# Performance work log

Hardware: AMD Instinct MI355X
Metric: run time of the kernel (lower is better)

The kernel has to match this reference:

```python
import jax, jax.numpy as jnp
import numpy as np

NUM_HEADS = 16

def setup_inputs() -> dict:
    key = jax.random.key(0)
    k1, k2, k3, k4 = jax.random.split(key, 4)
    B, S, D = 4, 4096, 2048
    scale = 1.0 / np.sqrt(D)
    return {
        "x": jax.random.normal(k1, (B, S, D), dtype=jnp.float32),
        "W_q": jax.random.normal(k2, (D, D), dtype=jnp.float32) * scale,
        "W_kv": jax.random.normal(k3, (D, D), dtype=jnp.float32) * scale,
        "W_o": jax.random.normal(k4, (D, D), dtype=jnp.float32) * scale,
    }

def _l2_normalize_complex(z):
    # torch.norm(z, dim=-1, keepdim=True) for complex: sqrt(sum |z|^2)
    n = jnp.sqrt(jnp.sum(jnp.abs(z) ** 2, axis=-1, keepdims=True))
    return z / n

def reference(x, W_q, W_kv, W_o):
    B, S, D = x.shape
    H = NUM_HEADS
    hd = D // H
    # Linear (no bias), torch convention: x @ W.T
    q = (x @ W_q.T).reshape(B, S, H, hd)
    kv = (x @ W_kv.T).reshape(B, S, H, hd)
    # HRR binding: FFT along head dim
    qf = jnp.fft.fft(q, axis=-1)
    kvf = jnp.fft.fft(kv, axis=-1)
    qf = _l2_normalize_complex(qf)
    kvf = _l2_normalize_complex(kvf)
    # causal=True: cumulative sum of bound key-values over sequence
    kvf = jnp.cumsum(kvf, axis=1)
    qv = qf * kvf
    values_hat = jnp.fft.ifft(qv, axis=-1).real.astype(x.dtype)
    values_hat = values_hat.reshape(B, S, D)
    return values_hat @ W_o.T
```

## Files before the change

### kernel.cpp

```cpp
#include <hip/hip_runtime.h>
#include <hip/hip_bf16.h>


typedef unsigned short u16;
typedef unsigned int u32;
typedef __attribute__((ext_vector_type(8))) short short8;
typedef __attribute__((ext_vector_type(4))) float f32x4;

__device__ __forceinline__ float bf2f(u16 u) {
  u32 x = ((u32)u) << 16;
  float f; __builtin_memcpy(&f, &x, 4); return f;
}
__device__ __forceinline__ u16 f2bf(float f) {
  __hip_bfloat16 h = __float2bfloat16(f);
  u16 u; __builtin_memcpy(&u, &h, 2); return u;
}
__device__ __forceinline__ u32 pack2(float a, float b) {
  return (u32)f2bf(a) | ((u32)f2bf(b) << 16);
}

#define GLD16(gp, lp)                                                        \
  __builtin_amdgcn_global_load_lds(                                          \
      (const __attribute__((address_space(1))) void*)(gp),                   \
      (__attribute__((address_space(3))) void*)(lp), 16, 0, 0)

__device__ __forceinline__ unsigned ldsoff(const void* p) {
  return (unsigned)(size_t)(const __attribute__((address_space(3))) char*)p;
}

#define DSR(dst, ad, im)                                                     \
  asm volatile("ds_read_b128 %0, %1 offset:%c2"                              \
               : "=v"(dst) : "v"(ad), "i"(im))

#define MM2(ACCE, X0, X1, Y0, Y1)                                            \
  ACCE = __builtin_amdgcn_mfma_f32_16x16x32_bf16(X0, Y0, ACCE, 0, 0, 0);     \
  ACCE = __builtin_amdgcn_mfma_f32_16x16x32_bf16(X1, Y1, ACCE, 0, 0, 0)

template <int EPI>
__global__ __launch_bounds__(512, 2) void gemm256(
    const u16* __restrict__ A, const u16* __restrict__ B, void* __restrict__ C,
    int N, int K) {
  __shared__ alignas(1024) char smem[131072];
  const int NT = K >> 6;
  const int ntn = N >> 8;
  const int nwg = gridDim.x;
  int wg = blockIdx.x;
  wg = (wg & 7) * (nwg >> 3) + (wg >> 3);
  const int bm = wg / ntn, bn = wg % ntn;
  const long rowBase = (long)bm << 8, colBase = (long)bn << 8;

  const int tid = threadIdx.x;
  const int w = tid >> 6, lane = tid & 63;
  const int quad = lane >> 4, l16 = lane & 15;
  const int wm = w >> 2, wn = w & 3;

  const int grow = w * 8 + (lane >> 3);
  const int gcol = ((lane & 7) * 8) ^ ((lane >> 4) << 4);
  const long voff = (long)grow * K + gcol;
  const u16* Abase = A + rowBase * (long)K;
  const u16* Bbase = B + colBase * (long)K;
  char* ldsA = smem;
  char* ldsB = smem + 65536;

#define STG_A(v, h)                                                          \
  do {                                                                       \
    char* d_ = ldsA + (((v)&1) << 15) + ((h) << 14) + (w << 10);             \
    GLD16(Abase + ((h) * 128L) * K + (long)(v) * 64 + voff, d_);             \
    GLD16(Abase + ((h) * 128L + 64) * K + (long)(v) * 64 + voff, d_ + 8192); \
  } while (0)
#define STG_B(v, h)                                                          \
  do {                                                                       \
    char* d_ = ldsB + (((v)&1) << 15) + ((h) << 14) + (w << 10);             \
    GLD16(Bbase + ((h) * 128L) * K + (long)(v) * 64 + voff, d_);             \
    GLD16(Bbase + ((h) * 128L + 64) * K + (long)(v) * 64 + voff, d_ + 8192); \
  } while (0)

  const int cb0 = (quad << 4) ^ (((l16 >> 1) & 3) << 5);
  const unsigned bA0 = ldsoff(ldsA + (wm * 128 + l16) * 128) + cb0;
  const unsigned bA1 = bA0 ^ 64;
  const unsigned bB0 = ldsoff(ldsB + (wn * 64 + l16) * 128) + cb0;
  const unsigned bB1 = bB0 ^ 64;

  short8 aL[8], aH[8], bl[4], bh[4];
  f32x4 acc[8][4] = {};

  STG_A(0, 0); STG_A(0, 1); STG_B(0, 0); STG_B(0, 1);
  STG_B(1, 0); STG_B(1, 1);
  asm volatile("s_waitcnt vmcnt(4)");
  __builtin_amdgcn_s_barrier();
  __builtin_amdgcn_sched_barrier(0);

#define Q0_BODY                                                              \
  _Pragma("unroll") for (int i = 0; i < 4; i++)                              \
    _Pragma("unroll") for (int j = 0; j < 2; j++) {                          \
      MM2(acc[i][j], aL[2*i], aL[2*i+1], bl[2*j], bl[2*j+1]);                \
    }
#define Q1_BODY                                                              \
  _Pragma("unroll") for (int i = 0; i < 4; i++)                              \
    _Pragma("unroll") for (int j = 0; j < 2; j++) {                          \
      MM2(acc[i][j+2], aL[2*i], aL[2*i+1], bh[2*j], bh[2*j+1]);              \
    }
#define Q2_BODY                                                              \
  _Pragma("unroll") for (int i = 0; i < 4; i++)                              \
    _Pragma("unroll") for (int j = 0; j < 2; j++) {                          \
      MM2(acc[i+4][j], aH[2*i], aH[2*i+1], bl[2*j], bl[2*j+1]);              \
    }
#define Q3_BODY                                                              \
  _Pragma("unroll") for (int i = 0; i < 4; i++)                              \
    _Pragma("unroll") for (int j = 0; j < 2; j++) {                          \
      MM2(acc[i+4][j+2], aH[2*i], aH[2*i+1], bh[2*j], bh[2*j+1]);            \
    }

#define RUN_TILE(uu, SA_, SB_, WAITSTMT)                                     \
  do {                                                                       \
    const unsigned bsel = ((uu) & 1) << 15;                                  \
    const unsigned aA0 = bA0 ^ bsel, aA1 = bA1 ^ bsel;                       \
    const unsigned aB0 = bB0 ^ bsel, aB1 = bB1 ^ bsel;                       \
                   \
    _Pragma("unroll") for (int i = 0; i < 4; i++) {                          \
      DSR(aL[2*i],   aA0, i * 2048);                                         \
      DSR(aL[2*i+1], aA1, i * 2048);                                         \
    }                                                                        \
    _Pragma("unroll") for (int j = 0; j < 2; j++) {                          \
      DSR(bl[2*j],   aB0, j * 2048);                                         \
      DSR(bl[2*j+1], aB1, j * 2048);                                         \
    }                                                                        \
    _Pragma("unroll") for (int j = 0; j < 2; j++) {                          \
      DSR(bh[2*j],   aB0, (j + 2) * 2048);                                   \
      DSR(bh[2*j+1], aB1, (j + 2) * 2048);                                   \
    }                                                                        \
    _Pragma("unroll") for (int i = 0; i < 4; i++) {                          \
      DSR(aH[2*i],   aA0, (i + 4) * 2048);                                   \
      DSR(aH[2*i+1], aA1, (i + 4) * 2048);                                   \
    }                                                                        \
    if (SA_) { STG_A((uu) + 1, 0); STG_A((uu) + 1, 1); }                     \
                       \
    asm volatile("s_waitcnt lgkmcnt(12)");                                   \
    __builtin_amdgcn_sched_barrier(0);                                       \
    __builtin_amdgcn_s_setprio(1);                                           \
    Q0_BODY                                                                  \
    __builtin_amdgcn_s_setprio(0);                                           \
                                   \
    asm volatile("s_waitcnt lgkmcnt(8)");                                    \
    __builtin_amdgcn_sched_barrier(0);                                       \
    __builtin_amdgcn_s_setprio(1);                                           \
    Q1_BODY                                                                  \
    __builtin_amdgcn_s_setprio(0);                                           \
    \
                       \
    __builtin_amdgcn_s_barrier();                                            \
    __builtin_amdgcn_sched_barrier(0);                                       \
    if (SB_) { STG_B((uu) + 2, 0); STG_B((uu) + 2, 1); }                     \
                                                          \
    asm volatile("s_waitcnt lgkmcnt(0)");                                    \
    __builtin_amdgcn_sched_barrier(0);                                       \
    __builtin_amdgcn_s_setprio(1);                                           \
    Q2_BODY                                                                  \
    Q3_BODY                                                                  \
    __builtin_amdgcn_s_setprio(0);                                           \
    WAITSTMT;                                                                \
    __builtin_amdgcn_s_barrier();                                            \
    __builtin_amdgcn_sched_barrier(0);                                       \
  } while (0)

  for (int u = 0; u < NT - 2; ++u) {
    RUN_TILE(u, true, true, asm volatile("s_waitcnt vmcnt(4)"));
  }
  RUN_TILE(NT - 2, true, false, asm volatile("s_waitcnt vmcnt(0)"));
  RUN_TILE(NT - 1, false, false, (void)0);
#undef RUN_TILE
#undef Q0_BODY
#undef Q1_BODY
#undef Q2_BODY
#undef Q3_BODY
#undef STG_A
#undef STG_B

  asm volatile("" ::: "memory");

  float scl[8][4];
#pragma unroll
  for (int i = 0; i < 8; i++)
#pragma unroll
    for (int r = 0; r < 4; r++) scl[i][r] = 1.0f;

  if (EPI == 2) {
    float* ssb = (float*)smem;
    __syncthreads();
#pragma unroll
    for (int i = 0; i < 8; i++)
#pragma unroll
      for (int r = 0; r < 4; r++) {
        float s = 0.f;
#pragma unroll
        for (int j = 0; j < 4; j++) { float v = acc[i][j][r]; s += v * v; }
        s += __shfl_xor(s, 1); s += __shfl_xor(s, 2);
        s += __shfl_xor(s, 4); s += __shfl_xor(s, 8);
        if (l16 == 0) ssb[((wm * 128 + i * 16 + quad * 4 + r) << 2) + wn] = s;
      }
    __syncthreads();
#pragma unroll
    for (int i = 0; i < 8; i++)
#pragma unroll
      for (int r = 0; r < 4; r++) {
        int row = wm * 128 + i * 16 + quad * 4 + r;
        float s = ssb[(row << 2) + (wn & 2)] + ssb[(row << 2) + (wn & 2) + 1];
        scl[i][r] = rsqrtf(128.0f * s);
      }
  }

#pragma unroll
  for (int i = 0; i < 8; i++) {
#pragma unroll
    for (int j = 0; j < 4; j++) {
      long row0 = rowBase + wm * 128 + i * 16 + quad * 4;
      long col = colBase + wn * 64 + j * 16 + l16;
#pragma unroll
      for (int r = 0; r < 4; r++) {
        float v = acc[i][j][r] * scl[i][r];
        long off = (row0 + r) * (long)N + col;
        if (EPI == 0) ((float*)C)[off] = v;
        else          ((u16*)C)[off] = f2bf(v);
      }
    }
  }
}

template <int EPI, bool FOLD>
__global__ __launch_bounds__(256, 2) void gemm_bt(
    const u16* __restrict__ A, const u16* __restrict__ B, void* __restrict__ C,
    int M, int N, int K, int lda) {
  const int ntiles = N >> 7;
  const int bid = blockIdx.x;
  const int bm = bid / ntiles, bn = bid % ntiles;
  const long rowBase = (long)bm * 128, colBase = (long)bn * 128;
  const long aOff = FOLD ? colBase : 0;
  const long bRowBase = FOLD ? 0 : colBase;

  __shared__ u16 As[128 * 32];
  __shared__ u16 Bs[128 * 32];
  __shared__ float ssbuf[128][2];

  const int tid = threadIdx.x;
  const int wave = tid >> 6, lane = tid & 63;
  const int quad = lane >> 4, l16 = lane & 15;
  const int waveRow = (wave >> 1) * 64, waveCol = (wave & 1) * 64;

  const int srow = lane >> 2, scol = (lane & 3) * 8;
  const u16* pa = A + (rowBase + wave * 32 + srow) * (long)lda + aOff + scol;
  const u16* pb = B + (bRowBase + wave * 32 + srow) * (long)K + scol;
  u16* lA0 = &As[(wave * 32) * 32];
  u16* lA1 = &As[(wave * 32 + 16) * 32];
  u16* lB0 = &Bs[(wave * 32) * 32];
  u16* lB1 = &Bs[(wave * 32 + 16) * 32];

  f32x4 acc[4][4] = {};

  for (int kt = 0; kt < K; kt += 32) {
    GLD16(pa + kt, lA0);
    GLD16(pa + kt + 16 * (long)lda, lA1);
    GLD16(pb + kt, lB0);
    GLD16(pb + kt + 16 * (long)K, lB1);
    __syncthreads();

    short8 af[4], bfr[4];
#pragma unroll
    for (int i = 0; i < 4; i++)
      af[i] = *(const short8*)&As[(waveRow + i * 16 + l16) * 32 + quad * 8];
#pragma unroll
    for (int j = 0; j < 4; j++)
      bfr[j] = *(const short8*)&Bs[(waveCol + j * 16 + l16) * 32 + quad * 8];
#pragma unroll
    for (int i = 0; i < 4; i++)
#pragma unroll
      for (int j = 0; j < 4; j++)
        acc[i][j] = __builtin_amdgcn_mfma_f32_16x16x32_bf16(af[i], bfr[j], acc[i][j], 0, 0, 0);
    __syncthreads();
  }

  float scl[4][4];
#pragma unroll
  for (int i = 0; i < 4; i++)
#pragma unroll
    for (int r = 0; r < 4; r++) scl[i][r] = 1.0f;

  if (EPI == 2) {
#pragma unroll
    for (int i = 0; i < 4; i++) {
#pragma unroll
      for (int r = 0; r < 4; r++) {
        float s = 0.f;
#pragma unroll
        for (int j = 0; j < 4; j++) { float v = acc[i][j][r]; s += v * v; }
#pragma unroll
        for (int m = 1; m < 16; m <<= 1) s += __shfl_xor(s, m);
        if (l16 == 0) ssbuf[waveRow + i * 16 + quad * 4 + r][wave & 1] = s;
      }
    }
    __syncthreads();
#pragma unroll
    for (int i = 0; i < 4; i++)
#pragma unroll
      for (int r = 0; r < 4; r++) {
        int row = waveRow + i * 16 + quad * 4 + r;
        scl[i][r] = rsqrtf(128.0f * (ssbuf[row][0] + ssbuf[row][1]));
      }
  }

#pragma unroll
  for (int i = 0; i < 4; i++) {
#pragma unroll
    for (int j = 0; j < 4; j++) {
      long row0 = rowBase + waveRow + i * 16 + quad * 4;
      long col = colBase + waveCol + j * 16 + l16;
#pragma unroll
      for (int r = 0; r < 4; r++) {
        float v = acc[i][j][r] * scl[i][r];
        long off = (row0 + r) * (long)N + col;
        if (EPI == 0) ((float*)C)[off] = v;
        else          ((u16*)C)[off] = f2bf(v);
      }
    }
  }
}

__global__ __launch_bounds__(256) void cast_f2b(const float* __restrict__ in,
                                                u16* __restrict__ out, int n4) {
  int i = blockIdx.x * 256 + threadIdx.x;
  if (i >= n4) return;
  float4 v = ((const float4*)in)[i];
  ushort4 u;
  u.x = f2bf(v.x); u.y = f2bf(v.y); u.z = f2bf(v.z); u.w = f2bf(v.w);
  ((ushort4*)out)[i] = u;
}

__global__ __launch_bounds__(256) void init_mats(u16* __restrict__ CSp,
                                                 u16* __restrict__ W2pT) {
  int idx = blockIdx.x * 256 + threadIdx.x;
  const float PI64 = 3.14159265358979323846f / 64.0f;
  if (idx < 16384) {
    int p = idx >> 7, n = idx & 127;
    int k = p >> 1;
    float v;
    if (p == 1) v = (n & 1) ? -1.f : 1.f;
    else {
      int t = (k * n) & 127;
      float ang = (float)t * PI64;
      v = (p & 1) ? -sinf(ang) : cosf(ang);
    }
    CSp[p * 128 + n] = f2bf(v);
  } else {
    int r = idx - 16384;
    int p = r >> 7, d = r & 127;
    int k = p >> 1;
    float v;
    if (p == 0) v = 1.0f / 128.0f;
    else if (p == 1) v = ((d & 1) ? -1.f : 1.f) / 128.0f;
    else {
      int t = (k * d) & 127;
      float ang = (float)t * PI64;
      v = ((p & 1) ? -2.f * sinf(ang) : 2.f * cosf(ang)) / 128.0f;
    }
    W2pT[p * 128 + d] = f2bf(v);
  }
}

__global__ __launch_bounds__(64) void scan_chunksum(const u16* __restrict__ F,
                                                    float* __restrict__ part) {
  int blk = blockIdx.x;
  int c = blk & 63, bh = blk >> 6;
  int h = bh & 15, b = bh >> 4;
  int l = threadIdx.x;
  float s0 = 0.f, s1 = 0.f;
  for (int t = c * 64; t < c * 64 + 64; ++t) {
    u32 u = ((const u32*)(F + ((long)(b * 4096 + t) * 32 + 16 + h) * 128))[l];
    s0 += bf2f((u16)(u & 0xffff));
    s1 += bf2f((u16)(u >> 16));
  }
  float2 w; w.x = s0; w.y = s1;
  ((float2*)part)[(long)blk * 64 + l] = w;
}

__global__ __launch_bounds__(128) void scan_exclusive(float* __restrict__ part) {
  int bh = blockIdx.x;
  int j = threadIdx.x;
  float run = 0.f;
  for (int c = 0; c < 64; ++c) {
    long idx = ((long)(bh * 64 + c)) * 128 + j;
    float v = part[idx];
    part[idx] = run;
    run += v;
  }
}

__global__ __launch_bounds__(64) void scan_main(const u16* __restrict__ F,
                                                u16* __restrict__ QV,
                                                const float* __restrict__ part) {
  int blk = blockIdx.x;
  int c = blk & 63, bh = blk >> 6;
  int h = bh & 15, b = bh >> 4;
  int l = threadIdx.x;
  float2 cc = ((const float2*)part)[(long)blk * 64 + l];
  float cr = cc.x, ci = cc.y;
  for (int t = c * 64; t < c * 64 + 64; ++t) {
    long m = (long)(b * 4096 + t);
    u32 ku = ((const u32*)(F + (m * 32 + 16 + h) * 128))[l];
    u32 qu = ((const u32*)(F + (m * 32 + h) * 128))[l];
    float kr = bf2f((u16)(ku & 0xffff)), ki = bf2f((u16)(ku >> 16));
    float qr = bf2f((u16)(qu & 0xffff)), qi = bf2f((u16)(qu >> 16));
    cr += kr; ci += ki;
    float vr, vi;
    if (l == 0) { vr = qr * cr; vi = qi * ci; }
    else { vr = qr * cr - qi * ci; vi = qr * ci + qi * cr; }
    ((u32*)(QV + (m * 16 + h) * 128))[l] = pack2(vr, vi);
  }
}

extern "C" void kernel_launch(void* const* d_in, const int* in_sizes, int n_in,
                              void* d_out, int out_size, void* d_ws, size_t ws_size,
                              hipStream_t stream) {
  const float* x   = (const float*)d_in[0];
  const float* Wq  = (const float*)d_in[1];
  const float* Wkv = (const float*)d_in[2];
  const float* Wo  = (const float*)d_in[3];
  float* out = (float*)d_out;

  const long M1 = 16384;
  const long D = 2048;
  const long R = M1 * 16;
  const long XE = M1 * D;
  const long WE = D * D;

  char* ws = (char*)d_ws;
  u16* qkh  = (u16*)(ws);
  u16* F    = (u16*)(ws + 134217728);
  u16* xb   = (u16*)(ws + 268435456);
  u16* wqkb = (u16*)(ws + 335544320);
  u16* wob  = (u16*)(ws + 352321536);
  u16* wo2  = (u16*)(ws + 360710144);
  u16* CSp  = (u16*)(ws + 369098752);
  u16* W2pT = (u16*)(ws + 369131520);
  float* part = (float*)(ws + 369164288);
  u16* QV = qkh;

  cast_f2b<<<(int)(XE / 4 / 256), 256, 0, stream>>>(x, xb, (int)(XE / 4));
  cast_f2b<<<(int)(WE / 4 / 256), 256, 0, stream>>>(Wq, wqkb, (int)(WE / 4));
  cast_f2b<<<(int)(WE / 4 / 256), 256, 0, stream>>>(Wkv, wqkb + WE, (int)(WE / 4));
  cast_f2b<<<(int)(WE / 4 / 256), 256, 0, stream>>>(Wo, wob, (int)(WE / 4));
  init_mats<<<128, 256, 0, stream>>>(CSp, W2pT);

  gemm_bt<1, true><<<16 * 16, 256, 0, stream>>>(wob, W2pT, wo2, 2048, 2048, 128, 2048);

  gemm256<2><<<(int)((M1 / 256) * (4096 / 256)), 512, 0, stream>>>(
      xb, wqkb, qkh, 4096, (int)D);

  gemm_bt<1, false><<<(int)(2 * R / 128), 256, 0, stream>>>(
      qkh, CSp, F, (int)(2 * R), 128, 128, 128);

  scan_chunksum<<<64 * 64, 64, 0, stream>>>(F, part);
  scan_exclusive<<<64, 128, 0, stream>>>(part);
  scan_main<<<64 * 64, 64, 0, stream>>>(F, QV, part);

  gemm256<0><<<(int)((M1 / 256) * (D / 256)), 512, 0, stream>>>(
      QV, wo2, out, (int)D, (int)D);
}
```

Measured before the change: 724.4 us.

## Fold per-head DFT into Q/KV weights to eliminate the separate FFT GEMM

Transposes and casts W_q and W_kv, then premultiplies them by the per-head DFT matrix (CSp) in a small GEMM with a transposed store. The main projection GEMM then writes the frequency-domain F directly, removing the large intermediate qkh write/read and the 2R×128 FFT GEMM pass. Because the pre-normalization values are no longer available, the L2-norm epilogue now rebuilds the complex-spectrum norm from the packed real-FFT layout (2S − E) instead of 128·sum. Small unroll pragmas are also added to the scan loops. The folded weights add one more bf16 rounding step before the projection, which may change accuracy.

```diff
diff --git a/kernel.cpp b/kernel.cpp
--- a/kernel.cpp
+++ b/kernel.cpp
@@ -116,7 +116,6 @@
     const unsigned bsel = ((uu) & 1) << 15;                                  \
     const unsigned aA0 = bA0 ^ bsel, aA1 = bA1 ^ bsel;                       \
     const unsigned aB0 = bB0 ^ bsel, aB1 = bB1 ^ bsel;                       \
-                   \
     _Pragma("unroll") for (int i = 0; i < 4; i++) {                          \
       DSR(aL[2*i],   aA0, i * 2048);                                         \
       DSR(aL[2*i+1], aA1, i * 2048);                                         \
@@ -134,24 +133,19 @@
       DSR(aH[2*i+1], aA1, (i + 4) * 2048);                                   \
     }                                                                        \
     if (SA_) { STG_A((uu) + 1, 0); STG_A((uu) + 1, 1); }                     \
-                       \
     asm volatile("s_waitcnt lgkmcnt(12)");                                   \
     __builtin_amdgcn_sched_barrier(0);                                       \
     __builtin_amdgcn_s_setprio(1);                                           \
     Q0_BODY                                                                  \
     __builtin_amdgcn_s_setprio(0);                                           \
-                                   \
     asm volatile("s_waitcnt lgkmcnt(8)");                                    \
     __builtin_amdgcn_sched_barrier(0);                                       \
     __builtin_amdgcn_s_setprio(1);                                           \
     Q1_BODY                                                                  \
     __builtin_amdgcn_s_setprio(0);                                           \
-    \
-                       \
     __builtin_amdgcn_s_barrier();                                            \
     __builtin_amdgcn_sched_barrier(0);                                       \
     if (SB_) { STG_B((uu) + 2, 0); STG_B((uu) + 2, 1); }                     \
-                                                          \
     asm volatile("s_waitcnt lgkmcnt(0)");                                    \
     __builtin_amdgcn_sched_barrier(0);                                       \
     __builtin_amdgcn_s_setprio(1);                                           \
@@ -194,9 +188,16 @@
         float s = 0.f;
 #pragma unroll
         for (int j = 0; j < 4; j++) { float v = acc[i][j][r]; s += v * v; }
-        s += __shfl_xor(s, 1); s += __shfl_xor(s, 2);
-        s += __shfl_xor(s, 4); s += __shfl_xor(s, 8);
-        if (l16 == 0) ssb[((wm * 128 + i * 16 + quad * 4 + r) << 2) + wn] = s;
+        float e = (l16 < 2) ? acc[i][0][r] * acc[i][0][r] : 0.f;
+        s += __shfl_xor(s, 1); e += __shfl_xor(e, 1);
+        s += __shfl_xor(s, 2); e += __shfl_xor(e, 2);
+        s += __shfl_xor(s, 4); e += __shfl_xor(e, 4);
+        s += __shfl_xor(s, 8); e += __shfl_xor(e, 8);
+        int row = wm * 128 + i * 16 + quad * 4 + r;
+        if (l16 == 0) {
+          ssb[(row << 3) + wn] = s;
+          if (!(wn & 1)) ssb[(row << 3) + 4 + (wn >> 1)] = e;
+        }
       }
     __syncthreads();
 #pragma unroll
@@ -204,8 +205,9 @@
 #pragma unroll
       for (int r = 0; r < 4; r++) {
         int row = wm * 128 + i * 16 + quad * 4 + r;
-        float s = ssb[(row << 2) + (wn & 2)] + ssb[(row << 2) + (wn & 2) + 1];
-        scl[i][r] = rsqrtf(128.0f * s);
+        float S = ssb[(row << 3) + (wn & 2)] + ssb[(row << 3) + (wn & 2) + 1];
+        float E = ssb[(row << 3) + 4 + (wn >> 1)];
+        scl[i][r] = rsqrtf(2.0f * S - E);
       }
   }
 
@@ -226,7 +228,7 @@
   }
 }
 
-template <int EPI, bool FOLD>
+template <int EPI, bool FOLD, bool TSTORE>
 __global__ __launch_bounds__(256, 2) void gemm_bt(
     const u16* __restrict__ A, const u16* __restrict__ B, void* __restrict__ C,
     int M, int N, int K, int lda) {
@@ -313,12 +315,19 @@
     for (int j = 0; j < 4; j++) {
       long row0 = rowBase + waveRow + i * 16 + quad * 4;
       long col = colBase + waveCol + j * 16 + l16;
-#pragma unroll
-      for (int r = 0; r < 4; r++) {
-        float v = acc[i][j][r] * scl[i][r];
-        long off = (row0 + r) * (long)N + col;
-        if (EPI == 0) ((float*)C)[off] = v;
-        else          ((u16*)C)[off] = f2bf(v);
+      if (TSTORE) {
+        uint2 v;
+        v.x = pack2(acc[i][j][0] * scl[i][0], acc[i][j][1] * scl[i][1]);
+        v.y = pack2(acc[i][j][2] * scl[i][2], acc[i][j][3] * scl[i][3]);
+        *(uint2*)((u16*)C + col * (long)M + row0) = v;
+      } else {
+#pragma unroll
+        for (int r = 0; r < 4; r++) {
+          float v = acc[i][j][r] * scl[i][r];
+          long off = (row0 + r) * (long)N + col;
+          if (EPI == 0) ((float*)C)[off] = v;
+          else          ((u16*)C)[off] = f2bf(v);
+        }
       }
     }
   }
@@ -332,6 +341,32 @@
   ushort4 u;
   u.x = f2bf(v.x); u.y = f2bf(v.y); u.z = f2bf(v.z); u.w = f2bf(v.w);
   ((ushort4*)out)[i] = u;
+}
+
+__global__ __launch_bounds__(256) void castT(const float* __restrict__ in,
+                                             u16* __restrict__ out, int co) {
+  __shared__ u16 tile[64][72];
+  const int bx = blockIdx.x & 31, by = blockIdx.x >> 5;
+  const int c0 = bx * 64, d0 = by * 64;
+  const int t = threadIdx.x;
+  const int rr = t >> 2, cc = (t & 3) * 16;
+  const float* ip = in + (long)(c0 + rr) * 2048 + d0 + cc;
+#pragma unroll
+  for (int e = 0; e < 4; e++) {
+    float4 v = ((const float4*)ip)[e];
+    tile[rr][cc + e * 4 + 0] = f2bf(v.x);
+    tile[rr][cc + e * 4 + 1] = f2bf(v.y);
+    tile[rr][cc + e * 4 + 2] = f2bf(v.z);
+    tile[rr][cc + e * 4 + 3] = f2bf(v.w);
+  }
+  __syncthreads();
+  u32 wb[8];
+#pragma unroll
+  for (int e = 0; e < 8; e++)
+    wb[e] = (u32)tile[cc + 2 * e][rr] | ((u32)tile[cc + 2 * e + 1][rr] << 16);
+  u32* op = (u32*)(out + (long)(d0 + rr) * 4096 + co + c0 + cc);
+#pragma unroll
+  for (int e = 0; e < 8; e++) op[e] = wb[e];
 }
 
 __global__ __launch_bounds__(256) void init_mats(u16* __restrict__ CSp,
@@ -372,6 +407,7 @@
   int h = bh & 15, b = bh >> 4;
   int l = threadIdx.x;
   float s0 = 0.f, s1 = 0.f;
+#pragma unroll 8
   for (int t = c * 64; t < c * 64 + 64; ++t) {
     u32 u = ((const u32*)(F + ((long)(b * 4096 + t) * 32 + 16 + h) * 128))[l];
     s0 += bf2f((u16)(u & 0xffff));
@@ -402,6 +438,7 @@
   int l = threadIdx.x;
   float2 cc = ((const float2*)part)[(long)blk * 64 + l];
   float cr = cc.x, ci = cc.y;
+#pragma unroll 4
   for (int t = c * 64; t < c * 64 + 64; ++t) {
     long m = (long)(b * 4096 + t);
     u32 ku = ((const u32*)(F + (m * 32 + 16 + h) * 128))[l];
@@ -427,35 +464,35 @@
 
   const long M1 = 16384;
   const long D = 2048;
-  const long R = M1 * 16;
   const long XE = M1 * D;
   const long WE = D * D;
 
   char* ws = (char*)d_ws;
-  u16* qkh  = (u16*)(ws);
+  u16* w2   = (u16*)(ws);
   u16* F    = (u16*)(ws + 134217728);
   u16* xb   = (u16*)(ws + 268435456);
-  u16* wqkb = (u16*)(ws + 335544320);
+  u16* wqkT = (u16*)(ws + 335544320);
   u16* wob  = (u16*)(ws + 352321536);
   u16* wo2  = (u16*)(ws + 360710144);
   u16* CSp  = (u16*)(ws + 369098752);
   u16* W2pT = (u16*)(ws + 369131520);
   float* part = (float*)(ws + 369164288);
-  u16* QV = qkh;
+  u16* QV = (u16*)(ws);
 
   cast_f2b<<<(int)(XE / 4 / 256), 256, 0, stream>>>(x, xb, (int)(XE / 4));
-  cast_f2b<<<(int)(WE / 4 / 256), 256, 0, stream>>>(Wq, wqkb, (int)(WE / 4));
-  cast_f2b<<<(int)(WE / 4 / 256), 256, 0, stream>>>(Wkv, wqkb + WE, (int)(WE / 4));
+  castT<<<1024, 256, 0, stream>>>(Wq, wqkT, 0);
+  castT<<<1024, 256, 0, stream>>>(Wkv, wqkT, 2048);
   cast_f2b<<<(int)(WE / 4 / 256), 256, 0, stream>>>(Wo, wob, (int)(WE / 4));
   init_mats<<<128, 256, 0, stream>>>(CSp, W2pT);
 
-  gemm_bt<1, true><<<16 * 16, 256, 0, stream>>>(wob, W2pT, wo2, 2048, 2048, 128, 2048);
+  gemm_bt<1, true, false><<<16 * 16, 256, 0, stream>>>(
+      wob, W2pT, wo2, 2048, 2048, 128, 2048);
+
+  gemm_bt<1, true, true><<<16 * 32, 256, 0, stream>>>(
+      wqkT, CSp, w2, 2048, 4096, 128, 4096);
 
   gemm256<2><<<(int)((M1 / 256) * (4096 / 256)), 512, 0, stream>>>(
-      xb, wqkb, qkh, 4096, (int)D);
-
-  gemm_bt<1, false><<<(int)(2 * R / 128), 256, 0, stream>>>(
-      qkh, CSp, F, (int)(2 * R), 128, 128, 128);
+      xb, w2, F, 4096, (int)D);
 
   scan_chunksum<<<64 * 64, 64, 0, stream>>>(F, part);
   scan_exclusive<<<64, 128, 0, stream>>>(part);
```

After: 695.2 us. 1.04x faster.
